# Kernel optimization log

Measured on AMD Instinct MI355X. Metric: run time of the kernel, lower is better.

Reference implementation:

```python
import jax, jax.numpy as jnp
import numpy as np

B, C, H, W = 8, 256, 48, 48


def setup_inputs() -> dict:
    key = jax.random.key(0)
    ks = jax.random.split(key, 16)
    d = {
        "rgb": jax.random.normal(ks[0], (B, C, H, W), dtype=jnp.float32),
        "t": jax.random.normal(ks[1], (B, C, H, W), dtype=jnp.float32),
    }
    names = ["wq1", "bq1", "wk1", "bk1", "wv1", "bv1",
             "wq2", "bq2", "wk2", "bk2", "wv2", "bv2"]
    for i, n in enumerate(names):
        if n.startswith("w"):
            d[n] = jax.random.normal(ks[2 + i], (C, C), dtype=jnp.float32) * 0.02
        else:
            d[n] = jax.random.normal(ks[2 + i], (C,), dtype=jnp.float32) * 0.02
    return d


def _cross_attention(x, y, wq, bq, wk, bk, wv, bv):
    # x, y: [b, c, h, w]; 1x1 convs == channel matmuls (ratio=1)
    b, c, h, w = x.shape
    xf = x.reshape(b, c, h * w)  # [b, c, n]
    yf = y.reshape(b, c, h * w)
    q = jnp.einsum('oi,bin->bno', wq, xf) + bq            # [b, n, c]
    k = jnp.einsum('oi,bin->bon', wk, yf) + bk[None, :, None]  # [b, c, n]
    v = jnp.einsum('oi,bin->bno', wv, yf) + bv            # [b, n, c]
    # unscaled attention, exactly as the torch module (no 1/sqrt(c))
    attn = jax.nn.softmax(jnp.einsum('bnc,bcm->bnm', q, k), axis=-1)  # [b, n, n]
    feat = q + jnp.einsum('bnm,bmc->bnc', attn, v)        # residual on q
    return feat.transpose(0, 2, 1).reshape(b, c, h, w)


def reference(rgb, t, wq1, bq1, wk1, bk1, wv1, bv1,
              wq2, bq2, wk2, bk2, wv2, bv2):
    feat_1 = _cross_attention(rgb, t, wq1, bq1, wk1, bk1, wv1, bv1)
    feat_2 = _cross_attention(t, rgb, wq2, bq2, wk2, bk2, wv2, bv2)
    out1 = rgb + feat_1
    out2 = t + feat_2
    return (out1, out2)
```

## Files before the change

### kernel.cpp

```cpp
#include <hip/hip_runtime.h>
#include <hip/hip_bf16.h>
#include <cstdint>

#define B_ 8
#define C_ 256
#define N_ 2304
#define XT_BYTES ((size_t)B_ * N_ * C_ * 2)
#define QK_BYTES ((size_t)16 * N_ * C_ * 2)
#define V_BYTES  ((size_t)16 * C_ * N_ * 2)

typedef __bf16 bf16x8 __attribute__((ext_vector_type(8)));
typedef float  f32x4  __attribute__((ext_vector_type(4)));
static_assert(sizeof(bf16x8) == 16, "");

__device__ __forceinline__ void gload16(const void* g, void* l) {
  __builtin_amdgcn_global_load_lds(
      reinterpret_cast<const __attribute__((address_space(1))) uint32_t*>(
          reinterpret_cast<uintptr_t>(g)),
      reinterpret_cast<__attribute__((address_space(3))) uint32_t*>(
          reinterpret_cast<uintptr_t>(l)),
      16, 0, 0);
}

__global__ __launch_bounds__(256) void k_transpose(
    const float* __restrict__ rgb, const float* __restrict__ tin,
    char* __restrict__ xT)
{
  const int nt = blockIdx.x;
  const int it = blockIdx.y;
  const int z  = blockIdx.z;
  const int src = z >> 3, b = z & 7;
  const float* __restrict__ in = (src ? tin : rgb) + (size_t)b * C_ * N_;
  char* __restrict__ out = xT + (size_t)src * XT_BYTES + (size_t)b * N_ * 512;
  const int i0 = it * 64, n0 = nt * 64;
  __shared__ float raw[64 * 65];
  const int t = threadIdx.x;
  const int rr = t >> 4;
  const int cc = t & 15;
#pragma unroll
  for (int j = 0; j < 4; ++j) {
    const int ii = rr + 16 * j;
    const float4 v = *(const float4*)(in + (size_t)(i0 + ii) * N_ + n0 + cc * 4);
    float* rp = &raw[ii * 65 + cc * 4];
    rp[0] = v.x; rp[1] = v.y; rp[2] = v.z; rp[3] = v.w;
  }
  __syncthreads();
#pragma unroll
  for (int k = 0; k < 4; ++k) {
    const int nl = rr + 16 * k;
    const int n = n0 + nl;
    union { __bf16 h[4]; uint2 u; } pk;
#pragma unroll
    for (int e = 0; e < 4; ++e)
      pk.h[e] = (__bf16)raw[(cc * 4 + e) * 65 + nl];
    const int cb = ((i0 + cc * 4) * 2) ^ ((n & 7) << 4);
    *(uint2*)(out + (size_t)n * 512 + cb) = pk.u;
  }
}

__global__ __launch_bounds__(256) void k_wcvt(
    const float* __restrict__ w0, const float* __restrict__ w1,
    const float* __restrict__ w2, const float* __restrict__ w3,
    const float* __restrict__ w4, const float* __restrict__ w5,
    char* __restrict__ Wb)
{
  const int widx = blockIdx.y;
  const float* w = widx == 0 ? w0 : widx == 1 ? w1 : widx == 2 ? w2
                 : widx == 3 ? w3 : widx == 4 ? w4 : w5;
  const int t = threadIdx.x;
  const int row = blockIdx.x * 8 + (t >> 5);
  const int c8 = (t & 31) * 8;
  const float4 v0 = *(const float4*)(w + row * 256 + c8);
  const float4 v1 = *(const float4*)(w + row * 256 + c8 + 4);
  union { __bf16 h[8]; uint4 u; } pk;
  pk.h[0] = (__bf16)v0.x; pk.h[1] = (__bf16)v0.y; pk.h[2] = (__bf16)v0.z; pk.h[3] = (__bf16)v0.w;
  pk.h[4] = (__bf16)v1.x; pk.h[5] = (__bf16)v1.y; pk.h[6] = (__bf16)v1.z; pk.h[7] = (__bf16)v1.w;
  const int cb = (c8 * 2) ^ ((row & 7) << 4);
  *(uint4*)(Wb + (size_t)(widx * 256 + row) * 512 + cb) = pk.u;
}

__global__ __launch_bounds__(256, 2) void k_proj_qk(
    const char* __restrict__ xT, const char* __restrict__ Wb,
    const float* __restrict__ bq1, const float* __restrict__ bk1,
    const float* __restrict__ bq2, const float* __restrict__ bk2,
    char* __restrict__ Qw, char* __restrict__ Kw)
{
  const int z = blockIdx.z;
  const int b = blockIdx.y;
  const int ntile = blockIdx.x >> 2, otile = blockIdx.x & 3;
  const int n0 = ntile * 128, o0 = otile * 64;
  const int srcT = (z == 1 || z == 2);
  const char* __restrict__ xp = xT + (size_t)srcT * XT_BYTES + (size_t)b * N_ * 512;
  const char* __restrict__ Wp = Wb + (size_t)z * C_ * 512;
  const float* __restrict__ bias = z == 0 ? bq1 : z == 1 ? bk1 : z == 2 ? bq2 : bk2;
  char* __restrict__ outp = ((z == 0 || z == 2) ? Qw : Kw)
                            + (size_t)((z >= 2 ? 8 : 0) + b) * N_ * 512;

  __shared__ alignas(16) char Alds[128 * 128];
  __shared__ alignas(16) char Wlds[64 * 128];
  const int t = threadIdx.x, lane = t & 63, wid = t >> 6;
  const int wm = wid >> 1, wn = wid & 1;
  const int lr = lane & 15, lk = lane >> 4;
  f32x4 acc[4][2] = {};

  for (int ko = 0; ko < 4; ++ko) {
    const int ib = ko * 128;
    __syncthreads();
#pragma unroll
    for (int s = 0; s < 4; ++s) {
      const int flat = s * 4096 + t * 16;
      *(uint4*)(Alds + flat) =
          *(const uint4*)(xp + (size_t)(n0 + (flat >> 7)) * 512 + ib + (flat & 127));
    }
#pragma unroll
    for (int s = 0; s < 2; ++s) {
      const int flat = s * 4096 + t * 16;
      *(uint4*)(Wlds + flat) =
          *(const uint4*)(Wp + (size_t)(o0 + (flat >> 7)) * 512 + ib + (flat & 127));
    }
    __syncthreads();
#pragma unroll
    for (int ks = 0; ks < 2; ++ks) {
      bf16x8 af[4], bfr[2];
#pragma unroll
      for (int mf = 0; mf < 4; ++mf) {
        const int row = wm * 64 + mf * 16 + lr;
        af[mf] = *(const bf16x8*)(Alds + row * 128 + ((ks * 64 + lk * 16) ^ ((row & 7) << 4)));
      }
#pragma unroll
      for (int nf = 0; nf < 2; ++nf) {
        const int row = wn * 32 + nf * 16 + lr;
        bfr[nf] = *(const bf16x8*)(Wlds + row * 128 + ((ks * 64 + lk * 16) ^ ((row & 7) << 4)));
      }
#pragma unroll
      for (int mf = 0; mf < 4; ++mf)
#pragma unroll
        for (int nf = 0; nf < 2; ++nf)
          acc[mf][nf] = __builtin_amdgcn_mfma_f32_16x16x32_bf16(af[mf], bfr[nf], acc[mf][nf], 0, 0, 0);
    }
  }
#pragma unroll
  for (int nf = 0; nf < 2; ++nf) {
    const int c = o0 + wn * 32 + nf * 16 + lr;
    const float bv = bias[c];
#pragma unroll
    for (int mf = 0; mf < 4; ++mf)
#pragma unroll
      for (int r = 0; r < 4; ++r) {
        const int n = n0 + wm * 64 + mf * 16 + lk * 4 + r;
        *(__bf16*)(outp + (size_t)n * 512 + ((c * 2) ^ ((n & 7) << 4))) =
            (__bf16)(acc[mf][nf][r] + bv);
      }
  }
}

__global__ __launch_bounds__(256, 2) void k_proj_v(
    const char* __restrict__ xT, const char* __restrict__ Wb,
    const float* __restrict__ bv1, const float* __restrict__ bv2,
    char* __restrict__ Vw)
{
  const int z = blockIdx.z;
  const int b = blockIdx.y;
  const int ntile = blockIdx.x >> 2, otile = blockIdx.x & 3;
  const int n0 = ntile * 128, o0 = otile * 64;
  const char* __restrict__ xp = xT + (size_t)(z == 0 ? 1 : 0) * XT_BYTES + (size_t)b * N_ * 512;
  const char* __restrict__ Wp = Wb + (size_t)(4 + z) * C_ * 512;
  const float* __restrict__ bias = z ? bv2 : bv1;
  char* __restrict__ outp = Vw + (size_t)(z * 8 + b) * C_ * 4608;

  __shared__ alignas(16) char Xlds[128 * 128];
  __shared__ alignas(16) char Wlds[64 * 128];
  const int t = threadIdx.x, lane = t & 63, wid = t >> 6;
  const int wm = wid >> 1, wn = wid & 1;
  const int lr = lane & 15, lk = lane >> 4;
  f32x4 acc[2][4] = {};

  for (int ko = 0; ko < 4; ++ko) {
    const int ib = ko * 128;
    __syncthreads();
#pragma unroll
    for (int s = 0; s < 4; ++s) {
      const int flat = s * 4096 + t * 16;
      *(uint4*)(Xlds + flat) =
          *(const uint4*)(xp + (size_t)(n0 + (flat >> 7)) * 512 + ib + (flat & 127));
    }
#pragma unroll
    for (int s = 0; s < 2; ++s) {
      const int flat = s * 4096 + t * 16;
      *(uint4*)(Wlds + flat) =
          *(const uint4*)(Wp + (size_t)(o0 + (flat >> 7)) * 512 + ib + (flat & 127));
    }
    __syncthreads();
#pragma unroll
    for (int ks = 0; ks < 2; ++ks) {
      bf16x8 af[2], bfr[4];
#pragma unroll
      for (int mf = 0; mf < 2; ++mf) {
        const int row = wm * 32 + mf * 16 + lr;
        af[mf] = *(const bf16x8*)(Wlds + row * 128 + ((ks * 64 + lk * 16) ^ ((row & 7) << 4)));
      }
#pragma unroll
      for (int nf = 0; nf < 4; ++nf) {
        const int row = wn * 64 + nf * 16 + lr;
        bfr[nf] = *(const bf16x8*)(Xlds + row * 128 + ((ks * 64 + lk * 16) ^ ((row & 7) << 4)));
      }
#pragma unroll
      for (int mf = 0; mf < 2; ++mf)
#pragma unroll
        for (int nf = 0; nf < 4; ++nf)
          acc[mf][nf] = __builtin_amdgcn_mfma_f32_16x16x32_bf16(af[mf], bfr[nf], acc[mf][nf], 0, 0, 0);
    }
  }
#pragma unroll
  for (int mf = 0; mf < 2; ++mf)
#pragma unroll
    for (int r = 0; r < 4; ++r) {
      const int o = o0 + wm * 32 + mf * 16 + lk * 4 + r;
      const float bv = bias[o];
#pragma unroll
      for (int nf = 0; nf < 4; ++nf) {
        const int n = n0 + wn * 64 + nf * 16 + lr;
        *(__bf16*)(outp + (size_t)o * 4608 + n * 2) =
            (__bf16)(acc[mf][nf][r] + bv);
      }
    }
}

__global__ __launch_bounds__(256, 3) void k_flash4(
    const char* __restrict__ Qw, const char* __restrict__ Kw, const char* __restrict__ Vw,
    const float* __restrict__ rgb, const float* __restrict__ tin,
    float* __restrict__ outp)
{
  const int F = blockIdx.x;
  const int xcd = F & 7, j = F >> 3;
  const int pair = xcd * 2 + (j >= 36 ? 1 : 0);
  const int qt = (j >= 36) ? j - 36 : j;
  const int a = pair >> 3, b = pair & 7;
  const char* __restrict__ Qp = Qw + (size_t)pair * N_ * 512;
  const char* __restrict__ Kp = Kw + (size_t)pair * N_ * 512;
  const char* __restrict__ Vp = Vw + (size_t)pair * C_ * 4608;
  const float* __restrict__ xsrc = (a ? tin : rgb) + (size_t)b * C_ * N_;
  float* __restrict__ op = outp + (size_t)(a * 8 + b) * C_ * N_;

  __shared__ alignas(16) char smem[69632];
  char* Pl = smem + 65536;

  const int t = threadIdx.x, lane = t & 63, w = t >> 6;
  const int lr = lane & 15, lk = lane >> 4;
  const int q0 = qt * 64;

  bf16x8 qf[8];
  {
    const int n = q0 + w * 16 + lr;
    const char* qrow = Qp + (size_t)n * 512;
    const int sw = (n & 7) << 4;
#pragma unroll
    for (int ks = 0; ks < 8; ++ks)
      qf[ks] = *(const bf16x8*)(qrow + ((ks * 64 + lk * 16) ^ sw));
  }

  f32x4 oacc[16] = {};
  float m_run[4], l_run[4];
#pragma unroll
  for (int r = 0; r < 4; ++r) { m_run[r] = -1e30f; l_run[r] = 0.f; }

#define STAGE_KV(T, CBUF)                                                     \
  {                                                                           \
    const char* Ks = Kp + (size_t)(T) * 32 * 512;                             \
    char* kd = smem + (CBUF) * 16384;                                         \
    _Pragma("unroll")                                                         \
    for (int s = 0; s < 4; ++s) {                                             \
      const int flat = s * 4096 + t * 16;                                     \
      gload16(Ks + flat, kd + flat);                                          \
    }                                                                         \
    const char* Vs = Vp + (size_t)(T) * 64;                                   \
    char* vd = smem + 32768 + (CBUF) * 16384;                                 \
    _Pragma("unroll")                                                         \
    for (int s = 0; s < 4; ++s) {                                             \
      const int flat = s * 4096 + t * 16;                                     \
      const int row = flat >> 6;                                              \
      const int slot = (flat >> 4) & 3;                                       \
      gload16(Vs + (size_t)row * 4608 + ((slot ^ (row & 3)) << 4), vd + flat);\
    }                                                                         \
  }

  STAGE_KV(0, 0);

  int c = 0;
  for (int kv = 0; kv < 72; ++kv) {
    __syncthreads();
    if (kv + 1 < 72) STAGE_KV(kv + 1, c ^ 1);

    const char* Kl = smem + c * 16384;
    const char* Vl = smem + 32768 + c * 16384;

    f32x4 s4[2] = {};
    __builtin_amdgcn_s_setprio(1);
#pragma unroll
    for (int mf = 0; mf < 2; ++mf) {
      const int row = mf * 16 + lr;
      const char* kr = Kl + row * 512;
      const int sw = (row & 7) << 4;
#pragma unroll
      for (int ks = 0; ks < 8; ++ks) {
        const bf16x8 kf = *(const bf16x8*)(kr + ((ks * 64 + lk * 16) ^ sw));
        s4[mf] = __builtin_amdgcn_mfma_f32_16x16x32_bf16(qf[ks], kf, s4[mf], 0, 0, 0);
      }
    }
    __builtin_amdgcn_s_setprio(0);

    float pmax[4];
#pragma unroll
    for (int r = 0; r < 4; ++r) {
      float m0 = fmaxf(s4[0][r], s4[1][r]);
      m0 = fmaxf(m0, __shfl_xor(m0, 1));
      m0 = fmaxf(m0, __shfl_xor(m0, 2));
      m0 = fmaxf(m0, __shfl_xor(m0, 4));
      m0 = fmaxf(m0, __shfl_xor(m0, 8));
      pmax[r] = m0;
    }
    bool need = false;
#pragma unroll
    for (int r = 0; r < 4; ++r) need |= (pmax[r] > m_run[r] + 8.f);
    if (__any(need)) {
#pragma unroll
      for (int r = 0; r < 4; ++r) {
        const float mn = fmaxf(m_run[r], pmax[r]);
        const float sc = __expf(m_run[r] - mn);
        m_run[r] = mn;
        l_run[r] *= sc;
#pragma unroll
        for (int cf = 0; cf < 16; ++cf) oacc[cf][r] *= sc;
      }
    }

    char* pw = Pl + w * 1024;
    {
      float psum[4] = {0.f, 0.f, 0.f, 0.f};
#pragma unroll
      for (int g = 0; g < 2; ++g)
#pragma unroll
        for (int r = 0; r < 4; ++r) {
          const float p = __expf(s4[g][r] - m_run[r]);
          psum[r] += p;
          const int row = lk * 4 + r;
          const int col = g * 16 + lr;
          *(__bf16*)(pw + row * 64 + ((col * 2) ^ ((row & 3) << 4))) = (__bf16)p;
        }
#pragma unroll
      for (int r = 0; r < 4; ++r) {
        float s0 = psum[r];
        s0 += __shfl_xor(s0, 1);
        s0 += __shfl_xor(s0, 2);
        s0 += __shfl_xor(s0, 4);
        s0 += __shfl_xor(s0, 8);
        l_run[r] += s0;
      }
    }

    __builtin_amdgcn_s_setprio(1);
    {
      const int slot = (lk ^ (lr & 3)) << 4;
      const bf16x8 pf = *(const bf16x8*)(pw + lr * 64 + slot);
#pragma unroll
      for (int cf = 0; cf < 16; ++cf) {
        const int row = cf * 16 + lr;
        const bf16x8 vf = *(const bf16x8*)(Vl + row * 64 + slot);
        oacc[cf] = __builtin_amdgcn_mfma_f32_16x16x32_bf16(pf, vf, oacc[cf], 0, 0, 0);
      }
    }
    __builtin_amdgcn_s_setprio(0);
    c ^= 1;
  }

  __syncthreads();
  {
    const char* Qsrc = Qp + (size_t)q0 * 512;
#pragma unroll
    for (int s = 0; s < 8; ++s) {
      const int flat = s * 4096 + t * 16;
      gload16(Qsrc + flat, smem + flat);
    }
  }
  __syncthreads();

  float inv[4];
#pragma unroll
  for (int r = 0; r < 4; ++r) inv[r] = 1.0f / l_run[r];
  const int nb = q0 + w * 16 + lk * 4;
  const int nl0 = w * 16 + lk * 4;
#pragma unroll
  for (int cf = 0; cf < 16; ++cf) {
    const int cc = cf * 16 + lr;
    const float4 xv = *(const float4*)(xsrc + (size_t)cc * N_ + nb);
    float vals[4];
#pragma unroll
    for (int r = 0; r < 4; ++r) {
      const int nl = nl0 + r;
      const float qv =
          (float)(*(const __bf16*)(smem + (size_t)nl * 512 + ((cc * 2) ^ ((nl & 7) << 4))));
      vals[r] = oacc[cf][r] * inv[r] + qv;
    }
    float4 ov;
    ov.x = vals[0] + xv.x; ov.y = vals[1] + xv.y;
    ov.z = vals[2] + xv.z; ov.w = vals[3] + xv.w;
    *(float4*)(op + (size_t)cc * N_ + nb) = ov;
  }
#undef STAGE_KV
}

extern "C" void kernel_launch(void* const* d_in, const int* in_sizes, int n_in,
                              void* d_out, int out_size, void* d_ws, size_t ws_size,
                              hipStream_t stream) {
  const float* rgb = (const float*)d_in[0];
  const float* tin = (const float*)d_in[1];
  const float* wq1 = (const float*)d_in[2];
  const float* bq1 = (const float*)d_in[3];
  const float* wk1 = (const float*)d_in[4];
  const float* bk1 = (const float*)d_in[5];
  const float* wv1 = (const float*)d_in[6];
  const float* bv1 = (const float*)d_in[7];
  const float* wq2 = (const float*)d_in[8];
  const float* bq2 = (const float*)d_in[9];
  const float* wk2 = (const float*)d_in[10];
  const float* bk2 = (const float*)d_in[11];
  const float* wv2 = (const float*)d_in[12];
  const float* bv2 = (const float*)d_in[13];

  char* ws = (char*)d_ws;
  char* xT = ws;
  char* Qw = ws + 2 * XT_BYTES;
  char* Kw = Qw + QK_BYTES;
  char* Vw = Kw + QK_BYTES;
  char* Wb = Vw + V_BYTES;

  k_transpose<<<dim3(36, 4, 16), 256, 0, stream>>>(rgb, tin, xT);
  k_wcvt<<<dim3(32, 6), 256, 0, stream>>>(wq1, wk1, wq2, wk2, wv1, wv2, Wb);
  k_proj_qk<<<dim3(72, 8, 4), 256, 0, stream>>>(xT, Wb, bq1, bk1, bq2, bk2, Qw, Kw);
  k_proj_v<<<dim3(72, 8, 2), 256, 0, stream>>>(xT, Wb, bv1, bv2, Vw);
  k_flash4<<<dim3(576), 256, 0, stream>>>(Qw, Kw, Vw, rgb, tin, (float*)d_out);
}
```

Baseline: 342.2 us.

## Compute S transposed so P stays in registers, dropping LDS round-trip for P

The QK^T MFMA now swaps its operands, so each lane holds scores for a single query row across 8 keys. The softmax max and sum then need only two cross-lane shuffles, and the bf16 P fragment can be packed directly into the A operand of the PV MFMA instead of being written to and re-read from shared memory. To match the new K ordering, V fragments are assembled from two 8-byte LDS reads, and row-wise rescale factors are broadcast with __shfl. The P scratch buffer is removed from LDS and the launch-bounds occupancy hint drops from 3 to 2, which may change register allocation and occupancy.

```diff
diff --git a/kernel.cpp b/kernel.cpp
--- a/kernel.cpp
+++ b/kernel.cpp
@@ -10,6 +10,7 @@
 #define V_BYTES  ((size_t)16 * C_ * N_ * 2)
 
 typedef __bf16 bf16x8 __attribute__((ext_vector_type(8)));
+typedef __bf16 bf16x4 __attribute__((ext_vector_type(4)));
 typedef float  f32x4  __attribute__((ext_vector_type(4)));
 static_assert(sizeof(bf16x8) == 16, "");
 
@@ -226,7 +227,7 @@
     }
 }
 
-__global__ __launch_bounds__(256, 3) void k_flash4(
+__global__ __launch_bounds__(256, 2) void k_flash5(
     const char* __restrict__ Qw, const char* __restrict__ Kw, const char* __restrict__ Vw,
     const float* __restrict__ rgb, const float* __restrict__ tin,
     float* __restrict__ outp)
@@ -242,8 +243,7 @@
   const float* __restrict__ xsrc = (a ? tin : rgb) + (size_t)b * C_ * N_;
   float* __restrict__ op = outp + (size_t)(a * 8 + b) * C_ * N_;
 
-  __shared__ alignas(16) char smem[69632];
-  char* Pl = smem + 65536;
+  __shared__ alignas(16) char smem[65536];
 
   const int t = threadIdx.x, lane = t & 63, w = t >> 6;
   const int lr = lane & 15, lk = lane >> 4;
@@ -260,9 +260,10 @@
   }
 
   f32x4 oacc[16] = {};
-  float m_run[4], l_run[4];
-#pragma unroll
-  for (int r = 0; r < 4; ++r) { m_run[r] = -1e30f; l_run[r] = 0.f; }
+  float m_run = -1e30f, l_run = 0.f;
+
+  const int vx0 = ((((lk >> 1) ^ (lr & 3)) << 4)) | ((lk & 1) << 3);
+  const int vx1 = (((2 + (lk >> 1)) ^ (lr & 3)) << 4) | ((lk & 1) << 3);
 
 #define STAGE_KV(T, CBUF)                                                     \
   {                                                                           \
@@ -294,80 +295,66 @@
     const char* Kl = smem + c * 16384;
     const char* Vl = smem + 32768 + c * 16384;
 
-    f32x4 s4[2] = {};
+    f32x4 st[2] = {};
     __builtin_amdgcn_s_setprio(1);
 #pragma unroll
-    for (int mf = 0; mf < 2; ++mf) {
-      const int row = mf * 16 + lr;
+    for (int sub = 0; sub < 2; ++sub) {
+      const int row = sub * 16 + lr;
       const char* kr = Kl + row * 512;
       const int sw = (row & 7) << 4;
 #pragma unroll
       for (int ks = 0; ks < 8; ++ks) {
         const bf16x8 kf = *(const bf16x8*)(kr + ((ks * 64 + lk * 16) ^ sw));
-        s4[mf] = __builtin_amdgcn_mfma_f32_16x16x32_bf16(qf[ks], kf, s4[mf], 0, 0, 0);
+        st[sub] = __builtin_amdgcn_mfma_f32_16x16x32_bf16(kf, qf[ks], st[sub], 0, 0, 0);
       }
     }
     __builtin_amdgcn_s_setprio(0);
 
-    float pmax[4];
-#pragma unroll
-    for (int r = 0; r < 4; ++r) {
-      float m0 = fmaxf(s4[0][r], s4[1][r]);
-      m0 = fmaxf(m0, __shfl_xor(m0, 1));
-      m0 = fmaxf(m0, __shfl_xor(m0, 2));
-      m0 = fmaxf(m0, __shfl_xor(m0, 4));
-      m0 = fmaxf(m0, __shfl_xor(m0, 8));
-      pmax[r] = m0;
-    }
-    bool need = false;
-#pragma unroll
-    for (int r = 0; r < 4; ++r) need |= (pmax[r] > m_run[r] + 8.f);
-    if (__any(need)) {
+    float pm = fmaxf(fmaxf(fmaxf(st[0][0], st[0][1]), fmaxf(st[0][2], st[0][3])),
+                     fmaxf(fmaxf(st[1][0], st[1][1]), fmaxf(st[1][2], st[1][3])));
+    pm = fmaxf(pm, __shfl_xor(pm, 16));
+    pm = fmaxf(pm, __shfl_xor(pm, 32));
+    if (__any(pm > m_run + 8.f)) {
+      const float mn = fmaxf(m_run, pm);
+      const float sc = __expf(m_run - mn);
+      m_run = mn;
+      l_run *= sc;
 #pragma unroll
       for (int r = 0; r < 4; ++r) {
-        const float mn = fmaxf(m_run[r], pmax[r]);
-        const float sc = __expf(m_run[r] - mn);
-        m_run[r] = mn;
-        l_run[r] *= sc;
-#pragma unroll
-        for (int cf = 0; cf < 16; ++cf) oacc[cf][r] *= sc;
-      }
-    }
-
-    char* pw = Pl + w * 1024;
-    {
-      float psum[4] = {0.f, 0.f, 0.f, 0.f};
-#pragma unroll
-      for (int g = 0; g < 2; ++g)
-#pragma unroll
-        for (int r = 0; r < 4; ++r) {
-          const float p = __expf(s4[g][r] - m_run[r]);
-          psum[r] += p;
-          const int row = lk * 4 + r;
-          const int col = g * 16 + lr;
-          *(__bf16*)(pw + row * 64 + ((col * 2) ^ ((row & 3) << 4))) = (__bf16)p;
-        }
+        const float sr = __shfl(sc, lk * 4 + r);
+#pragma unroll
+        for (int cf = 0; cf < 16; ++cf) oacc[cf][r] *= sr;
+      }
+    }
+    float p[8];
+    float ps = 0.f;
+#pragma unroll
+    for (int s2 = 0; s2 < 2; ++s2)
 #pragma unroll
       for (int r = 0; r < 4; ++r) {
-        float s0 = psum[r];
-        s0 += __shfl_xor(s0, 1);
-        s0 += __shfl_xor(s0, 2);
-        s0 += __shfl_xor(s0, 4);
-        s0 += __shfl_xor(s0, 8);
-        l_run[r] += s0;
-      }
-    }
+        const float e = __expf(st[s2][r] - m_run);
+        p[s2 * 4 + r] = e;
+        ps += e;
+      }
+    ps += __shfl_xor(ps, 16);
+    ps += __shfl_xor(ps, 32);
+    l_run += ps;
+
+    bf16x8 pa;
+#pragma unroll
+    for (int jj = 0; jj < 8; ++jj) pa[jj] = (__bf16)p[jj];
 
     __builtin_amdgcn_s_setprio(1);
-    {
-      const int slot = (lk ^ (lr & 3)) << 4;
-      const bf16x8 pf = *(const bf16x8*)(pw + lr * 64 + slot);
-#pragma unroll
-      for (int cf = 0; cf < 16; ++cf) {
-        const int row = cf * 16 + lr;
-        const bf16x8 vf = *(const bf16x8*)(Vl + row * 64 + slot);
-        oacc[cf] = __builtin_amdgcn_mfma_f32_16x16x32_bf16(pf, vf, oacc[cf], 0, 0, 0);
-      }
+    const char* vb = Vl + lr * 64;
+#pragma unroll
+    for (int cf = 0; cf < 16; ++cf) {
+      const char* vr = vb + cf * 1024;
+      const bf16x4 a0 = *(const bf16x4*)(vr + vx0);
+      const bf16x4 a1 = *(const bf16x4*)(vr + vx1);
+      bf16x8 vf;
+#pragma unroll
+      for (int jj = 0; jj < 4; ++jj) { vf[jj] = a0[jj]; vf[4 + jj] = a1[jj]; }
+      oacc[cf] = __builtin_amdgcn_mfma_f32_16x16x32_bf16(pa, vf, oacc[cf], 0, 0, 0);
     }
     __builtin_amdgcn_s_setprio(0);
     c ^= 1;
@@ -384,9 +371,11 @@
   }
   __syncthreads();
 
+  const float rl = 1.0f / l_run;
   float inv[4];
 #pragma unroll
-  for (int r = 0; r < 4; ++r) inv[r] = 1.0f / l_run[r];
+  for (int r = 0; r < 4; ++r) inv[r] = __shfl(rl, lk * 4 + r);
+
   const int nb = q0 + w * 16 + lk * 4;
   const int nl0 = w * 16 + lk * 4;
 #pragma unroll
@@ -438,5 +427,5 @@
   k_wcvt<<<dim3(32, 6), 256, 0, stream>>>(wq1, wk1, wq2, wk2, wv1, wv2, Wb);
   k_proj_qk<<<dim3(72, 8, 4), 256, 0, stream>>>(xT, Wb, bq1, bk1, bq2, bk2, Qw, Kw);
   k_proj_v<<<dim3(72, 8, 2), 256, 0, stream>>>(xT, Wb, bv1, bv2, Vw);
-  k_flash4<<<dim3(576), 256, 0, stream>>>(Qw, Kw, Vw, rgb, tin, (float*)d_out);
-}
+  k_flash5<<<dim3(576), 256, 0, stream>>>(Qw, Kw, Vw, rgb, tin, (float*)d_out);
+}
```

New measurement: 445.2 us. 1.3x slower.
